# Kernel tuning notes

Hardware: AMD Instinct MI355X
Metric: run time of the kernel (lower is better)

## Reference

```python
import jax, jax.numpy as jnp
import numpy as np

B, D, H = 8192, 256, 512


def setup_inputs() -> dict:
    key = jax.random.key(0)
    ks = jax.random.split(key, 25)
    inp = {
        "x": jax.random.normal(ks[0], (B, D), jnp.float32),
        "h_t": jax.random.normal(ks[1], (B, H), jnp.float32),
        "h_s": jax.random.normal(ks[2], (B, H), jnp.float32),
        "c_t": jax.random.normal(ks[3], (B, H), jnp.float32),
        "c_s": jax.random.normal(ks[4], (B, H), jnp.float32),
    }
    names = ["Ui", "Wti", "Wsi", "bi", "Us", "Wts", "Wss", "bs",
             "Ut", "Wtt", "Wst", "bt", "Uo", "Wto", "Wso", "bo",
             "Uc", "Wtc", "Wsc", "bc"]
    shapes = {"U": (D, H), "W": (H, H), "b": (H,)}
    scale = 0.02  # keep activations in a sane range
    for i, n in enumerate(names):
        s = shapes["U"] if n[0] == "U" else (shapes["b"] if n[0] == "b" else shapes["W"])
        inp[n] = jax.random.normal(ks[5 + i], s, jnp.float32) * scale
    return inp


def reference(x, h_t, h_s, c_t, c_s,
              Ui, Wti, Wsi, bi, Us, Wts, Wss, bs,
              Ut, Wtt, Wst, bt, Uo, Wto, Wso, bo,
              Uc, Wtc, Wsc, bc):
    # Fuse the 15 small GEMMs into 3 concatenated GEMMs: [B,D]@[D,5H] etc.
    U = jnp.concatenate([Ui, Us, Ut, Uo, Uc], axis=1)      # [D, 5H]
    Wt = jnp.concatenate([Wti, Wts, Wtt, Wto, Wtc], axis=1)  # [H, 5H]
    Ws = jnp.concatenate([Wsi, Wss, Wst, Wso, Wsc], axis=1)  # [H, 5H]
    b = jnp.concatenate([bi, bs, bt, bo, bc])                # [5H]
    gates = x @ U + h_t @ Wt + h_s @ Ws + b                  # [B, 5H]
    g_i, g_fs, g_ft, g_o, g_c = jnp.split(gates, 5, axis=1)
    i_n = jax.nn.sigmoid(g_i)
    f_s_n = jax.nn.sigmoid(g_fs)
    f_t_n = jax.nn.sigmoid(g_ft)
    o_n = jax.nn.sigmoid(g_o)
    c_n = jnp.tanh(g_c)
    c_h = i_n * c_n + f_t_n * c_t + f_s_n * c_s
    h = o_n * jnp.tanh(c_h)
    return (h, c_h)
```

## Files before the change

kernel.cpp:

```cpp
#include <hip/hip_runtime.h>
#include <hip/hip_bf16.h>
#include <cstdint>
#include <cstddef>

#define B_  8192
#define D_  256
#define H_  512
#define K_  1280
#define N_  2560
#define NT_ 160

typedef short short8 __attribute__((ext_vector_type(8)));
typedef float f32x4  __attribute__((ext_vector_type(4)));

__device__ __forceinline__ float sigf(float x)     { return 1.f / (1.f + __expf(-x)); }
__device__ __forceinline__ float tanhfast(float x) { return 1.f - 2.f / (__expf(2.f * x) + 1.f); }

struct WPtrs {
    const float* U[5];
    const float* Wt[5];
    const float* Ws[5];
};

__global__ void prep_kernel(const float* __restrict__ x, const float* __restrict__ ht,
                            const float* __restrict__ hs, WPtrs p,
                            __hip_bfloat16* __restrict__ A, __hip_bfloat16* __restrict__ WT) {
    __shared__ __hip_bfloat16 tile[64][72];
    int bid = blockIdx.x;
    if (bid < 5120) {
        int t = bid * 256 + threadIdx.x;
        int idx8 = t * 8;
        int b = idx8 / K_;
        int k = idx8 - b * K_;
        const float* src;
        if (k < D_)            src = x  + (size_t)b * D_ + k;
        else if (k < D_ + H_)  src = ht + (size_t)b * H_ + (k - D_);
        else                   src = hs + (size_t)b * H_ + (k - D_ - H_);
        f32x4 v0 = *(const f32x4*)(src);
        f32x4 v1 = *(const f32x4*)(src + 4);
        union { short8 s; __hip_bfloat16 h[8]; } o;
        o.h[0] = __float2bfloat16(v0[0]); o.h[1] = __float2bfloat16(v0[1]);
        o.h[2] = __float2bfloat16(v0[2]); o.h[3] = __float2bfloat16(v0[3]);
        o.h[4] = __float2bfloat16(v1[0]); o.h[5] = __float2bfloat16(v1[1]);
        o.h[6] = __float2bfloat16(v1[2]); o.h[7] = __float2bfloat16(v1[3]);
        *(short8*)(A + idx8) = o.s;
    } else {
        int bid2 = bid - 5120;
        int hblk = bid2 & 7;
        int kblk = (bid2 >> 3) % 20;
        int g    = bid2 / 160;
        int k0 = kblk * 64;
        int h0 = hblk * 64;
        const float* src; int kl0;
        if (k0 < 256)      { src = p.U[g];  kl0 = k0; }
        else if (k0 < 768) { src = p.Wt[g]; kl0 = k0 - 256; }
        else               { src = p.Ws[g]; kl0 = k0 - 768; }
        int tid = threadIdx.x;
        int tk = tid >> 6;
        int th = tid & 63;
        for (int r = 0; r < 16; ++r) {
            int kl = r * 4 + tk;
            tile[kl][th] = __float2bfloat16(src[(size_t)(kl0 + kl) * H_ + h0 + th]);
        }
        __syncthreads();
        for (int r = 0; r < 16; ++r) {
            int hl = r * 4 + tk;
            int h  = h0 + hl;
            int np = (h >> 4) * 80 + g * 16 + (h & 15);
            WT[(size_t)np * K_ + k0 + th] = tile[th][hl];
        }
    }
}

#define GLD16(gp, lp)                                                              \
    __builtin_amdgcn_global_load_lds(                                              \
        (const __attribute__((address_space(1))) unsigned int*)(gp),               \
        (__attribute__((address_space(3))) unsigned int*)(lp), 16, 0, 0)

__global__ __launch_bounds__(512, 4) void gemm_fused_kernel(
    const __hip_bfloat16* __restrict__ A, const __hip_bfloat16* __restrict__ WT,
    const float* __restrict__ ct, const float* __restrict__ cs,
    const float* __restrict__ bi, const float* __restrict__ bfs,
    const float* __restrict__ bft, const float* __restrict__ bo,
    const float* __restrict__ bc, float* __restrict__ out) {
    __shared__ alignas(16) unsigned short sA[128 * 32];
    __shared__ alignas(16) unsigned short sB[NT_ * 32];

    int tid = threadIdx.x;
    int m0 = blockIdx.x * 128;
    int n0 = blockIdx.y * NT_;
    int wid  = tid >> 6, lane = tid & 63;
    int wm   = wid >> 1;
    int wn   = wid & 1;
    int quad = lane >> 4, l15 = lane & 15;

    int h = (blockIdx.y * 2 + wn) * 16 + l15;
    float Bi = bi[h], Bfs = bfs[h], Bft = bft[h], Bo = bo[h], Bc = bc[h];

    f32x4 acc[2][5];
#pragma unroll
    for (int i = 0; i < 2; ++i)
#pragma unroll
        for (int j = 0; j < 5; ++j)
            acc[i][j] = (f32x4){0.f, 0.f, 0.f, 0.f};

    int srow = tid >> 2;
    int scol = (tid & 3) * 8;
    const __hip_bfloat16* Abase = A  + (size_t)(m0 + srow) * K_ + scol;
    const __hip_bfloat16* Bbase = WT + (size_t)(n0 + srow) * K_ + scol;
    unsigned short* AsDst = sA + tid * 8;
    unsigned short* BsDst = sB + tid * 8;

    for (int k0 = 0; k0 < K_; k0 += 32) {
        GLD16(Abase + k0, AsDst);
        GLD16(Bbase + k0, BsDst);
        if (tid < 128)
            GLD16(Bbase + k0 + (size_t)128 * K_, BsDst + 4096);
        __syncthreads();

        short8 a[2], b[5];
#pragma unroll
        for (int i = 0; i < 2; ++i)
            a[i] = *(const short8*)(sA + (wm * 32 + i * 16 + l15) * 32 + quad * 8);
#pragma unroll
        for (int j = 0; j < 5; ++j)
            b[j] = *(const short8*)(sB + (wn * 80 + j * 16 + l15) * 32 + quad * 8);
#pragma unroll
        for (int j = 0; j < 5; ++j)
#pragma unroll
            for (int i = 0; i < 2; ++i)
                acc[i][j] = __builtin_amdgcn_mfma_f32_16x16x32_bf16(a[i], b[j], acc[i][j], 0, 0, 0);
        __syncthreads();
    }

#pragma unroll
    for (int i = 0; i < 2; ++i) {
        int row0 = m0 + wm * 32 + i * 16 + quad * 4;
#pragma unroll
        for (int r = 0; r < 4; ++r) {
            size_t idx = (size_t)(row0 + r) * H_ + h;
            float i_n  = sigf(acc[i][0][r] + Bi);
            float fs_n = sigf(acc[i][1][r] + Bfs);
            float ft_n = sigf(acc[i][2][r] + Bft);
            float o_n  = sigf(acc[i][3][r] + Bo);
            float c_n  = tanhfast(acc[i][4][r] + Bc);
            float ch   = i_n * c_n + ft_n * ct[idx] + fs_n * cs[idx];
            out[idx] = o_n * tanhfast(ch);
            out[(size_t)B_ * H_ + idx] = ch;
        }
    }
}

struct AllW {
    const float* U[5];
    const float* Wt[5];
    const float* Ws[5];
    const float* bias[5];
};

__global__ __launch_bounds__(512) void fallback_kernel(const float* __restrict__ x,
                                                       const float* __restrict__ ht,
                                                       const float* __restrict__ hs,
                                                       const float* __restrict__ ct,
                                                       const float* __restrict__ cs,
                                                       AllW w, float* __restrict__ out) {
    __shared__ float arow[K_];
    int b = blockIdx.x;
    int h = threadIdx.x;
    for (int k = h; k < K_; k += 512) {
        float v;
        if (k < D_)           v = x[b * D_ + k];
        else if (k < D_ + H_) v = ht[b * H_ + k - D_];
        else                  v = hs[b * H_ + k - D_ - H_];
        arow[k] = v;
    }
    __syncthreads();
    float g[5];
    for (int gi = 0; gi < 5; ++gi) {
        float s = w.bias[gi][h];
        const float* U = w.U[gi];
        for (int k = 0; k < D_; ++k) s += arow[k] * U[(size_t)k * H_ + h];
        const float* Wt = w.Wt[gi];
        for (int k = 0; k < H_; ++k) s += arow[D_ + k] * Wt[(size_t)k * H_ + h];
        const float* Ws = w.Ws[gi];
        for (int k = 0; k < H_; ++k) s += arow[D_ + H_ + k] * Ws[(size_t)k * H_ + h];
        g[gi] = s;
    }
    int idx = b * H_ + h;
    float i_n = sigf(g[0]), fs_n = sigf(g[1]), ft_n = sigf(g[2]), o_n = sigf(g[3]);
    float c_n = tanhfast(g[4]);
    float ch  = i_n * c_n + ft_n * ct[idx] + fs_n * cs[idx];
    out[idx] = o_n * tanhfast(ch);
    out[(size_t)B_ * H_ + idx] = ch;
}

extern "C" void kernel_launch(void* const* d_in, const int* in_sizes, int n_in,
                              void* d_out, int out_size, void* d_ws, size_t ws_size,
                              hipStream_t stream) {
    const float* x  = (const float*)d_in[0];
    const float* ht = (const float*)d_in[1];
    const float* hs = (const float*)d_in[2];
    const float* ct = (const float*)d_in[3];
    const float* cs = (const float*)d_in[4];

    WPtrs wp;
    AllW  aw;
    const float* bias[5];
    for (int g = 0; g < 5; ++g) {
        wp.U[g]  = (const float*)d_in[5 + g * 4 + 0];
        wp.Wt[g] = (const float*)d_in[5 + g * 4 + 1];
        wp.Ws[g] = (const float*)d_in[5 + g * 4 + 2];
        bias[g]  = (const float*)d_in[5 + g * 4 + 3];
        aw.U[g] = wp.U[g]; aw.Wt[g] = wp.Wt[g]; aw.Ws[g] = wp.Ws[g]; aw.bias[g] = bias[g];
    }
    float* out = (float*)d_out;

    size_t szA = (size_t)B_ * K_ * 2;
    size_t szW = (size_t)N_ * K_ * 2;

    if (ws_size >= szA + szW) {
        __hip_bfloat16* Abf = (__hip_bfloat16*)d_ws;
        __hip_bfloat16* WT  = (__hip_bfloat16*)((char*)d_ws + szA);

        prep_kernel<<<5120 + 800, 256, 0, stream>>>(x, ht, hs, wp, Abf, WT);
        gemm_fused_kernel<<<dim3(B_ / 128, N_ / NT_), 512, 0, stream>>>(
            Abf, WT, ct, cs, bias[0], bias[1], bias[2], bias[3], bias[4], out);
    } else {
        fallback_kernel<<<B_, 512, 0, stream>>>(x, ht, hs, ct, cs, aw, out);
    }
}
```

Measured before the change: 242.6 us.

## Switch GEMM to 32x32x16 MFMA with larger per-wave tiles and swizzled LDS

The fused GEMM moves from 16x16x32 to 32x32x16 bf16 MFMA, doubles the N tile to 320 and uses 256-thread blocks. Each wave now owns a 64x160 output tile, and the weight layout in the prep kernel is regrouped into 32-column gate groups to match. LDS chunks are XOR-swizzled to avoid bank conflicts on the fragment reads. The aim is more arithmetic per LDS and global load and fewer MFMA issues, at the cost of many more accumulator registers (160 floats per lane) and lower occupancy.

```diff
diff --git a/kernel.cpp b/kernel.cpp
--- a/kernel.cpp
+++ b/kernel.cpp
@@ -8,10 +8,11 @@
 #define H_  512
 #define K_  1280
 #define N_  2560
-#define NT_ 160
-
-typedef short short8 __attribute__((ext_vector_type(8)));
-typedef float f32x4  __attribute__((ext_vector_type(4)));
+#define NT_ 320
+
+typedef short short8  __attribute__((ext_vector_type(8)));
+typedef float f32x4   __attribute__((ext_vector_type(4)));
+typedef float f32x16  __attribute__((ext_vector_type(16)));
 
 __device__ __forceinline__ float sigf(float x)     { return 1.f / (1.f + __expf(-x)); }
 __device__ __forceinline__ float tanhfast(float x) { return 1.f - 2.f / (__expf(2.f * x) + 1.f); }
@@ -66,7 +67,7 @@
         for (int r = 0; r < 16; ++r) {
             int hl = r * 4 + tk;
             int h  = h0 + hl;
-            int np = (h >> 4) * 80 + g * 16 + (h & 15);
+            int np = (h >> 5) * 160 + g * 32 + (h & 31);
             WT[(size_t)np * K_ + k0 + th] = tile[th][hl];
         }
     }
@@ -77,7 +78,7 @@
         (const __attribute__((address_space(1))) unsigned int*)(gp),               \
         (__attribute__((address_space(3))) unsigned int*)(lp), 16, 0, 0)
 
-__global__ __launch_bounds__(512, 4) void gemm_fused_kernel(
+__global__ __launch_bounds__(256, 2) void gemm_fused_kernel(
     const __hip_bfloat16* __restrict__ A, const __hip_bfloat16* __restrict__ WT,
     const float* __restrict__ ct, const float* __restrict__ cs,
     const float* __restrict__ bi, const float* __restrict__ bfs,
@@ -92,53 +93,80 @@
     int wid  = tid >> 6, lane = tid & 63;
     int wm   = wid >> 1;
     int wn   = wid & 1;
-    int quad = lane >> 4, l15 = lane & 15;
-
-    int h = (blockIdx.y * 2 + wn) * 16 + l15;
+    int half = lane >> 5, l31 = lane & 31;
+
+    int hg = blockIdx.y * 2 + wn;
+    int h  = hg * 32 + l31;
     float Bi = bi[h], Bfs = bfs[h], Bft = bft[h], Bo = bo[h], Bc = bc[h];
 
-    f32x4 acc[2][5];
+    f32x16 acc[2][5];
 #pragma unroll
     for (int i = 0; i < 2; ++i)
 #pragma unroll
         for (int j = 0; j < 5; ++j)
-            acc[i][j] = (f32x4){0.f, 0.f, 0.f, 0.f};
-
-    int srow = tid >> 2;
-    int scol = (tid & 3) * 8;
-    const __hip_bfloat16* Abase = A  + (size_t)(m0 + srow) * K_ + scol;
-    const __hip_bfloat16* Bbase = WT + (size_t)(n0 + srow) * K_ + scol;
-    unsigned short* AsDst = sA + tid * 8;
-    unsigned short* BsDst = sB + tid * 8;
+            acc[i][j] = (f32x16)(0.f);
+
+    const __hip_bfloat16* aSrc[2]; unsigned short* aDst[2];
+#pragma unroll
+    for (int i = 0; i < 2; ++i) {
+        int c = tid + 256 * i;
+        int row = c >> 2, pos = c & 3;
+        int kc = pos ^ ((row >> 1) & 3);
+        aSrc[i] = A + (size_t)(m0 + row) * K_ + kc * 8;
+        aDst[i] = sA + c * 8;
+    }
+    const __hip_bfloat16* bSrc[5]; unsigned short* bDst[5];
+#pragma unroll
+    for (int i = 0; i < 5; ++i) {
+        int c = tid + 256 * i;
+        int row = c >> 2, pos = c & 3;
+        int kc = pos ^ ((row >> 1) & 3);
+        bSrc[i] = WT + (size_t)(n0 + row) * K_ + kc * 8;
+        bDst[i] = sB + c * 8;
+    }
+
+    int arow[2], brow[5];
+#pragma unroll
+    for (int i = 0; i < 2; ++i) arow[i] = wm * 64 + i * 32 + l31;
+#pragma unroll
+    for (int j = 0; j < 5; ++j) brow[j] = wn * 160 + j * 32 + l31;
 
     for (int k0 = 0; k0 < K_; k0 += 32) {
-        GLD16(Abase + k0, AsDst);
-        GLD16(Bbase + k0, BsDst);
-        if (tid < 128)
-            GLD16(Bbase + k0 + (size_t)128 * K_, BsDst + 4096);
+#pragma unroll
+        for (int i = 0; i < 2; ++i) GLD16(aSrc[i] + k0, aDst[i]);
+#pragma unroll
+        for (int i = 0; i < 5; ++i) GLD16(bSrc[i] + k0, bDst[i]);
         __syncthreads();
 
-        short8 a[2], b[5];
-#pragma unroll
-        for (int i = 0; i < 2; ++i)
-            a[i] = *(const short8*)(sA + (wm * 32 + i * 16 + l15) * 32 + quad * 8);
-#pragma unroll
-        for (int j = 0; j < 5; ++j)
-            b[j] = *(const short8*)(sB + (wn * 80 + j * 16 + l15) * 32 + quad * 8);
-#pragma unroll
-        for (int j = 0; j < 5; ++j)
-#pragma unroll
-            for (int i = 0; i < 2; ++i)
-                acc[i][j] = __builtin_amdgcn_mfma_f32_16x16x32_bf16(a[i], b[j], acc[i][j], 0, 0, 0);
+#pragma unroll
+        for (int ks = 0; ks < 2; ++ks) {
+            short8 a[2], b[5];
+#pragma unroll
+            for (int i = 0; i < 2; ++i) {
+                int pos = (ks * 2 + half) ^ ((arow[i] >> 1) & 3);
+                a[i] = *(const short8*)(sA + arow[i] * 32 + pos * 8);
+            }
+#pragma unroll
+            for (int j = 0; j < 5; ++j) {
+                int pos = (ks * 2 + half) ^ ((brow[j] >> 1) & 3);
+                b[j] = *(const short8*)(sB + brow[j] * 32 + pos * 8);
+            }
+#pragma unroll
+            for (int j = 0; j < 5; ++j)
+#pragma unroll
+                for (int i = 0; i < 2; ++i)
+                    acc[i][j] = __builtin_amdgcn_mfma_f32_32x32x16_bf16(a[i], b[j], acc[i][j], 0, 0, 0);
+        }
         __syncthreads();
     }
 
 #pragma unroll
     for (int i = 0; i < 2; ++i) {
-        int row0 = m0 + wm * 32 + i * 16 + quad * 4;
-#pragma unroll
-        for (int r = 0; r < 4; ++r) {
-            size_t idx = (size_t)(row0 + r) * H_ + h;
+        int rbase = m0 + wm * 64 + i * 32 + 4 * half;
+#pragma unroll
+        for (int r = 0; r < 16; ++r) {
+            int row = rbase + (r & 3) + 8 * (r >> 2);
+            size_t idx = (size_t)row * H_ + h;
             float i_n  = sigf(acc[i][0][r] + Bi);
             float fs_n = sigf(acc[i][1][r] + Bfs);
             float ft_n = sigf(acc[i][2][r] + Bft);
@@ -223,7 +251,7 @@
         __hip_bfloat16* WT  = (__hip_bfloat16*)((char*)d_ws + szA);
 
         prep_kernel<<<5120 + 800, 256, 0, stream>>>(x, ht, hs, wp, Abf, WT);
-        gemm_fused_kernel<<<dim3(B_ / 128, N_ / NT_), 512, 0, stream>>>(
+        gemm_fused_kernel<<<dim3(B_ / 128, N_ / NT_), 256, 0, stream>>>(
             Abf, WT, ct, cs, bias[0], bias[1], bias[2], bias[3], bias[4], out);
     } else {
         fallback_kernel<<<B_, 512, 0, stream>>>(x, ht, hs, ct, cs, aw, out);
```

Measured after the change: 235.6 us. -2.9%, faster.
